# Optimization experiments

Hardware: AMD Instinct MI355X
Metric: run time of the kernel (lower is better)

## Reference

```python
import jax, jax.numpy as jnp
import numpy as np

EMBED_DIM = 1024
ATTN_DIM = 128
B, S = 4, 2048


def setup_inputs() -> dict:
    key = jax.random.key(0)
    k1, k2, k3, k4 = jax.random.split(key, 4)
    embedded = jax.random.normal(k1, (B, S, EMBED_DIM), dtype=jnp.float32)
    # torch nn.Linear weights are [out_features, in_features]
    scale = 1.0 / np.sqrt(EMBED_DIM)
    Wk = jax.random.uniform(k2, (ATTN_DIM, EMBED_DIM), dtype=jnp.float32, minval=-scale, maxval=scale)
    Wq = jax.random.uniform(k3, (ATTN_DIM, EMBED_DIM), dtype=jnp.float32, minval=-scale, maxval=scale)
    Wv = jax.random.uniform(k4, (ATTN_DIM, EMBED_DIM), dtype=jnp.float32, minval=-scale, maxval=scale)
    return {"embedded": embedded, "Wk": Wk, "Wq": Wq, "Wv": Wv}


def reference(embedded, Wk, Wq, Wv):
    # projections (no bias): x @ W.T
    k = jnp.einsum('bse,ae->bsa', embedded, Wk)  # [B,S,A]
    q = jnp.einsum('bse,ae->bsa', embedded, Wq)
    v = jnp.einsum('bse,ae->bsa', embedded, Wv)
    ad = k.shape[-1]
    scores = jnp.einsum('bqa,bka->bqk', q, k) / jnp.sqrt(jnp.float32(ad))  # [B,S,S]
    causal = jnp.tril(jnp.ones((scores.shape[1], scores.shape[1]), dtype=bool))
    scores = jnp.where(causal, scores, -jnp.inf)
    probs = jax.nn.softmax(scores, axis=-1)
    out = jnp.einsum('bqk,bka->bqa', probs, v)
    return jnp.round(out, 4)
```

## Files before the change

kernel.cpp:

```cpp
#include <hip/hip_runtime.h>
#include <hip/hip_bf16.h>
#include <math.h>

#define B 4
#define S 2048
#define E 1024
#define A 128
#define CHUNK 256
#define NCHMAX 8

typedef __attribute__((ext_vector_type(8))) short short8;
typedef __attribute__((ext_vector_type(4))) float floatx4;

static __device__ __forceinline__ short f2bf(float f) {
  union { float f; unsigned u; } c;
  c.f = f;
  unsigned r = (c.u + 0x7fffu + ((c.u >> 16) & 1u)) >> 16;
  return (short)r;
}
static __device__ __forceinline__ unsigned f2bf2(float x, float y) {
  __hip_bfloat162 h = __float22bfloat162_rn(float2{x, y});
  union { __hip_bfloat162 h; unsigned u; } c;
  c.h = h;
  return c.u;
}

__global__ __launch_bounds__(256) void proj_gemm(
    const float* __restrict__ X,
    const float* __restrict__ Wq,
    const float* __restrict__ Wk,
    const float* __restrict__ Wv,
    short* __restrict__ Qbf,
    short* __restrict__ Kbf,
    short* __restrict__ Vt) {
  __shared__ short As[64 * 64];
  __shared__ short Bs[128 * 64];

  const int m0 = blockIdx.x * 64;
  const int which = blockIdx.y;
  const float* Wpb = (which == 0) ? Wq : (which == 1) ? Wk : Wv;

  const int tid = threadIdx.x;
  const int wave = tid >> 6;
  const int lane = tid & 63;
  const int mh = wave & 1;
  const int nh = wave >> 1;
  const int l16 = lane & 15;
  const int quad = lane >> 4;

  int xbase[4], wbase[4], aoff[4], boff[4];
#pragma unroll
  for (int i = 0; i < 4; ++i) {
    const int fa = tid + i * 256;
    const int arow = fa >> 4, ac4 = fa & 15;
    xbase[i] = (m0 + arow) * E + ac4 * 4;
    aoff[i] = arow * 64 + (((ac4 >> 1) ^ (arow & 7)) << 3) + ((ac4 & 1) << 2);
    const int fb = tid + i * 256;
    const int brow = fb >> 3, bc8 = fb & 7;
    wbase[i] = brow * E + bc8 * 8;
    boff[i] = brow * 64 + ((bc8 ^ (brow & 7)) << 3);
  }

  int arb[2], brb[4], swz[2];
#pragma unroll
  for (int ms = 0; ms < 2; ++ms) arb[ms] = (mh * 32 + ms * 16 + l16) * 64;
#pragma unroll
  for (int nt = 0; nt < 4; ++nt) brb[nt] = (nh * 64 + nt * 16 + l16) * 64;
#pragma unroll
  for (int ks = 0; ks < 2; ++ks) swz[ks] = (((ks * 4 + quad) ^ (l16 & 7)) << 3);

  floatx4 acc[2][4] = {};
  float4 apl0[4], apl1[4];
  float4 bpl0[4][2], bpl1[4][2];

#pragma unroll
  for (int i = 0; i < 4; ++i) {
    apl0[i] = *(const float4*)&X[xbase[i]];
    bpl0[i][0] = *(const float4*)&Wpb[wbase[i]];
    bpl0[i][1] = *(const float4*)&Wpb[wbase[i] + 4];
    apl1[i] = *(const float4*)&X[xbase[i] + 64];
    bpl1[i][0] = *(const float4*)&Wpb[wbase[i] + 64];
    bpl1[i][1] = *(const float4*)&Wpb[wbase[i] + 68];
  }

#define PROJ_BODY(APL, BPL, KNEXT)                                            \
  do {                                                                        \
    __syncthreads();                                                          \
    _Pragma("unroll") for (int i = 0; i < 4; ++i) {                           \
      uint2 pk; pk.x = f2bf2(APL[i].x, APL[i].y);                             \
      pk.y = f2bf2(APL[i].z, APL[i].w);                                       \
      *(uint2*)&As[aoff[i]] = pk;                                             \
      uint4 pb;                                                               \
      pb.x = f2bf2(BPL[i][0].x, BPL[i][0].y);                                 \
      pb.y = f2bf2(BPL[i][0].z, BPL[i][0].w);                                 \
      pb.z = f2bf2(BPL[i][1].x, BPL[i][1].y);                                 \
      pb.w = f2bf2(BPL[i][1].z, BPL[i][1].w);                                 \
      *(uint4*)&Bs[boff[i]] = pb;                                             \
    }                                                                         \
    __syncthreads();                                                          \
    if ((KNEXT) < E) {                                                        \
      _Pragma("unroll") for (int i = 0; i < 4; ++i) {                         \
        APL[i] = *(const float4*)&X[xbase[i] + (KNEXT)];                      \
        BPL[i][0] = *(const float4*)&Wpb[wbase[i] + (KNEXT)];                 \
        BPL[i][1] = *(const float4*)&Wpb[wbase[i] + (KNEXT) + 4];             \
      }                                                                       \
    }                                                                         \
    short8 afr[2][2], bfr[4][2];                                              \
    _Pragma("unroll") for (int ms = 0; ms < 2; ++ms)                          \
      _Pragma("unroll") for (int ks = 0; ks < 2; ++ks)                        \
        afr[ms][ks] = *(const short8*)&As[arb[ms] + swz[ks]];                 \
    _Pragma("unroll") for (int nt = 0; nt < 4; ++nt)                          \
      _Pragma("unroll") for (int ks = 0; ks < 2; ++ks)                        \
        bfr[nt][ks] = *(const short8*)&Bs[brb[nt] + swz[ks]];                 \
    _Pragma("unroll") for (int ms = 0; ms < 2; ++ms)                          \
      _Pragma("unroll") for (int nt = 0; nt < 4; ++nt)                        \
        _Pragma("unroll") for (int ks = 0; ks < 2; ++ks)                      \
          acc[ms][nt] = __builtin_amdgcn_mfma_f32_16x16x32_bf16(              \
              afr[ms][ks], bfr[nt][ks], acc[ms][nt], 0, 0, 0);                \
  } while (0)

  for (int k0 = 0; k0 < E; k0 += 128) {
    PROJ_BODY(apl0, bpl0, k0 + 128);
    PROJ_BODY(apl1, bpl1, k0 + 192);
  }
#undef PROJ_BODY

  const float qscale = 0.08838834764831845f;
#pragma unroll
  for (int ms = 0; ms < 2; ++ms) {
#pragma unroll
    for (int nt = 0; nt < 4; ++nt) {
      const int n = nh * 64 + nt * 16 + l16;
      const int mbase = m0 + mh * 32 + ms * 16 + quad * 4;
      if (which == 2) {
        const int b = mbase >> 11, s = mbase & (S - 1);
        short4 p;
        p.x = f2bf(acc[ms][nt][0]); p.y = f2bf(acc[ms][nt][1]);
        p.z = f2bf(acc[ms][nt][2]); p.w = f2bf(acc[ms][nt][3]);
        *(short4*)&Vt[((size_t)b * A + n) * S + s] = p;
      } else {
        short* Outp = (which == 0) ? Qbf : Kbf;
        const float sc = (which == 0) ? qscale : 1.0f;
#pragma unroll
        for (int r = 0; r < 4; ++r)
          Outp[(size_t)(mbase + r) * A + n] = f2bf(acc[ms][nt][r] * sc);
      }
    }
  }
}

__global__ __launch_bounds__(256) void attn_part(
    const short* __restrict__ Qbf,
    const short* __restrict__ Kbf,
    const short* __restrict__ Vt,
    float* __restrict__ Opart,
    float* __restrict__ Lpart) {
  __shared__ short Ks[64 * 128];
  __shared__ short Vs[128 * 64];
  __shared__ short Ps[4][16 * 64];

  const int rev = (int)gridDim.x - 1 - (int)blockIdx.x;
  const int qt = rev >> 3;
  const int chunk = rev & 7;
  const int b = qt >> 5;
  const int q0 = (qt & 31) << 6;
  const int nk = q0 + 64;
  const int kstart = chunk * CHUNK;
  if (kstart >= nk) return;
  const int kend = min(kstart + CHUNK, nk);

  const int tid = threadIdx.x;
  const int wave = tid >> 6;
  const int lane = tid & 63;
  const int l16 = lane & 15;
  const int quad = lane >> 4;

  int kgb[4], vgb[4], kwoff[4], vwoff[4];
#pragma unroll
  for (int i = 0; i < 4; ++i) {
    const int f = tid + i * 256;
    const int krow = f >> 4, kc8 = f & 15;
    kgb[i] = krow * A + kc8 * 8;
    kwoff[i] = krow * 128 + ((kc8 ^ (krow & 7)) << 3);
    const int vrow = f >> 3, vc8 = f & 7;
    vgb[i] = vrow * S + vc8 * 8;
    vwoff[i] = vrow * 64 + ((vc8 ^ (vrow & 7)) << 3);
  }

  int swz[4];
#pragma unroll
  for (int ks = 0; ks < 4; ++ks) swz[ks] = (((ks * 4 + quad) ^ (l16 & 7)) << 3);

  int pwoff[4][4];
#pragma unroll
  for (int nt = 0; nt < 4; ++nt)
#pragma unroll
    for (int r = 0; r < 4; ++r) {
      const int row = quad * 4 + r;
      const int slot = nt * 2 + (l16 >> 3);
      pwoff[nt][r] = row * 64 + ((slot ^ (row & 7)) << 3) + (l16 & 7);
    }

  short8 qfr[4];
  {
    const size_t qrow = (size_t)(b * S + q0 + wave * 16 + l16);
#pragma unroll
    for (int ks = 0; ks < 4; ++ks)
      qfr[ks] = *(const short8*)&Qbf[qrow * A + ks * 32 + quad * 8];
  }

  float l_acc[4] = {0.f, 0.f, 0.f, 0.f};
  floatx4 oacc[8] = {};

  const int myrow = q0 + wave * 16 + quad * 4;
  const short* Kbase = Kbf + (size_t)b * S * A;
  const short* Vbase = Vt + (size_t)b * A * S;

  short8 kplf[4], vplf[4];
#pragma unroll
  for (int i = 0; i < 4; ++i) {
    kplf[i] = *(const short8*)&Kbase[kstart * A + kgb[i]];
    vplf[i] = *(const short8*)&Vbase[vgb[i] + kstart];
  }

  for (int j0 = kstart; j0 < kend; j0 += 64) {
    __syncthreads();
#pragma unroll
    for (int i = 0; i < 4; ++i) {
      *(short8*)&Ks[kwoff[i]] = kplf[i];
      *(short8*)&Vs[vwoff[i]] = vplf[i];
    }
    __syncthreads();

    if (j0 + 64 < kend) {
#pragma unroll
      for (int i = 0; i < 4; ++i) {
        kplf[i] = *(const short8*)&Kbase[(j0 + 64) * A + kgb[i]];
        vplf[i] = *(const short8*)&Vbase[vgb[i] + j0 + 64];
      }
    }

    floatx4 sc[4];
#pragma unroll
    for (int nt = 0; nt < 4; ++nt) {
      floatx4 c = {};
#pragma unroll
      for (int ks = 0; ks < 4; ++ks) {
        const short8 bfr = *(const short8*)&Ks[(nt * 16 + l16) * 128 + swz[ks]];
        c = __builtin_amdgcn_mfma_f32_16x16x32_bf16(qfr[ks], bfr, c, 0, 0, 0);
      }
      sc[nt] = c;
    }

#pragma unroll
    for (int nt = 0; nt < 4; ++nt) {
      const int key = j0 + nt * 16 + l16;
#pragma unroll
      for (int r = 0; r < 4; ++r) {
        const float p = (key > myrow + r) ? 0.f : __expf(sc[nt][r]);
        sc[nt][r] = p;
        l_acc[r] += p;
      }
    }

#pragma unroll
    for (int nt = 0; nt < 4; ++nt)
#pragma unroll
      for (int r = 0; r < 4; ++r)
        Ps[wave][pwoff[nt][r]] = f2bf(sc[nt][r]);

    short8 pfr[2];
#pragma unroll
    for (int ks = 0; ks < 2; ++ks)
      pfr[ks] = *(const short8*)&Ps[wave][l16 * 64 + swz[ks]];

#pragma unroll
    for (int nt = 0; nt < 8; ++nt) {
#pragma unroll
      for (int ks = 0; ks < 2; ++ks) {
        const short8 vfr = *(const short8*)&Vs[(nt * 16 + l16) * 64 + swz[ks]];
        oacc[nt] = __builtin_amdgcn_mfma_f32_16x16x32_bf16(pfr[ks], vfr, oacc[nt], 0, 0, 0);
      }
    }
  }

  const int slot = qt * NCHMAX + chunk;
  float* op = Opart + (size_t)slot * 64 * 128;
  const int lr = wave * 16 + quad * 4;
#pragma unroll
  for (int nt = 0; nt < 8; ++nt)
#pragma unroll
    for (int r = 0; r < 4; ++r)
      op[(lr + r) * 128 + nt * 16 + l16] = oacc[nt][r];

#pragma unroll
  for (int r = 0; r < 4; ++r) {
    float l = l_acc[r];
    l += __shfl_xor(l, 1);
    l += __shfl_xor(l, 2);
    l += __shfl_xor(l, 4);
    l += __shfl_xor(l, 8);
    if (l16 == 0) Lpart[slot * 64 + lr + r] = l;
  }
}

__global__ __launch_bounds__(256) void attn_reduce(
    const float* __restrict__ Opart,
    const float* __restrict__ Lpart,
    float* __restrict__ Out) {
  const int qt = blockIdx.x >> 2;
  const int quarter = blockIdx.x & 3;
  const int b = qt >> 5;
  const int q0 = (qt & 31) << 6;
  const int nch = (q0 + 64 + CHUNK - 1) / CHUNK;

  const int tid = threadIdx.x;
  const int lr = quarter * 16 + (tid >> 4);
  const int c0 = (tid & 15) * 8;

  float ltot = 0.f;
  for (int c = 0; c < nch; ++c) ltot += Lpart[(qt * NCHMAX + c) * 64 + lr];
  const float inv = 1.f / ltot;

  float4 acc[2] = {};
  for (int c = 0; c < nch; ++c) {
    const float4* op = (const float4*)
        (Opart + ((size_t)(qt * NCHMAX + c) * 64 + lr) * 128 + c0);
#pragma unroll
    for (int i = 0; i < 2; ++i) {
      const float4 v = op[i];
      acc[i].x += v.x; acc[i].y += v.y; acc[i].z += v.z; acc[i].w += v.w;
    }
  }

  float4* o = (float4*)(Out + (size_t)(b * S + q0 + lr) * A + c0);
#pragma unroll
  for (int i = 0; i < 2; ++i) {
    float4 v = acc[i];
    v.x *= inv; v.y *= inv; v.z *= inv; v.w *= inv;
    o[i] = v;
  }
}

extern "C" void kernel_launch(void* const* d_in, const int* in_sizes, int n_in,
                              void* d_out, int out_size, void* d_ws, size_t ws_size,
                              hipStream_t stream) {
  const float* X  = (const float*)d_in[0];
  const float* Wk = (const float*)d_in[1];
  const float* Wq = (const float*)d_in[2];
  const float* Wv = (const float*)d_in[3];
  float* Out = (float*)d_out;

  const size_t qkv_elems = (size_t)B * S * A;
  short* Qbf = (short*)d_ws;
  short* Kbf = Qbf + qkv_elems;
  short* Vt  = Kbf + qkv_elems;
  float* Opart = (float*)(Vt + qkv_elems);
  float* Lpart = Opart + (size_t)1024 * 64 * 128;

  dim3 pgrid(B * S / 64, 3);
  proj_gemm<<<pgrid, 256, 0, stream>>>(X, Wq, Wk, Wv, Qbf, Kbf, Vt);
  attn_part<<<(B * S / 64) * NCHMAX, 256, 0, stream>>>(Qbf, Kbf, Vt, Opart, Lpart);
  attn_reduce<<<B * S / 64 * 4, 256, 0, stream>>>(Opart, Lpart, Out);
}
```

Baseline: 124.1 us.

## Accumulate split-K attention partials with atomics instead of per-chunk buffers

Attention partial outputs and row sums are now accumulated into a single unnormalized output buffer with float atomicAdd, instead of being written to per-chunk slots and summed in the reduce kernel. The accumulators are zeroed inside the projection kernel. Query tiles that need only one key chunk write normalized output directly and skip the reduce. This cuts partial-buffer traffic and reduce work, at the cost of atomic contention and a nondeterministic summation order.

```diff
diff --git a/kernel.cpp b/kernel.cpp
--- a/kernel.cpp
+++ b/kernel.cpp
@@ -32,7 +32,9 @@
     const float* __restrict__ Wv,
     short* __restrict__ Qbf,
     short* __restrict__ Kbf,
-    short* __restrict__ Vt) {
+    short* __restrict__ Vt,
+    float* __restrict__ Ounn,
+    float* __restrict__ Ltot) {
   __shared__ short As[64 * 64];
   __shared__ short Bs[128 * 64];
 
@@ -41,6 +43,15 @@
   const float* Wpb = (which == 0) ? Wq : (which == 1) ? Wk : Wv;
 
   const int tid = threadIdx.x;
+
+  if (which == 0) {
+    const float4 z = {0.f, 0.f, 0.f, 0.f};
+    float4* zb = (float4*)&Ounn[(size_t)m0 * A];
+#pragma unroll
+    for (int i = 0; i < 8; ++i) zb[tid + i * 256] = z;
+    if (tid < 64) Ltot[m0 + tid] = 0.f;
+  }
+
   const int wave = tid >> 6;
   const int lane = tid & 63;
   const int mh = wave & 1;
@@ -153,8 +164,9 @@
     const short* __restrict__ Qbf,
     const short* __restrict__ Kbf,
     const short* __restrict__ Vt,
-    float* __restrict__ Opart,
-    float* __restrict__ Lpart) {
+    float* __restrict__ Ounn,
+    float* __restrict__ Ltot,
+    float* __restrict__ Out) {
   __shared__ short Ks[64 * 128];
   __shared__ short Vs[128 * 64];
   __shared__ short Ps[4][16 * 64];
@@ -168,6 +180,7 @@
   const int kstart = chunk * CHUNK;
   if (kstart >= nk) return;
   const int kend = min(kstart + CHUNK, nk);
+  const int nch = (nk + CHUNK - 1) / CHUNK;
 
   const int tid = threadIdx.x;
   const int wave = tid >> 6;
@@ -284,15 +297,8 @@
     }
   }
 
-  const int slot = qt * NCHMAX + chunk;
-  float* op = Opart + (size_t)slot * 64 * 128;
   const int lr = wave * 16 + quad * 4;
-#pragma unroll
-  for (int nt = 0; nt < 8; ++nt)
-#pragma unroll
-    for (int r = 0; r < 4; ++r)
-      op[(lr + r) * 128 + nt * 16 + l16] = oacc[nt][r];
-
+  float lsum[4];
 #pragma unroll
   for (int r = 0; r < 4; ++r) {
     float l = l_acc[r];
@@ -300,43 +306,59 @@
     l += __shfl_xor(l, 2);
     l += __shfl_xor(l, 4);
     l += __shfl_xor(l, 8);
-    if (l16 == 0) Lpart[slot * 64 + lr + r] = l;
+    lsum[r] = l;
+  }
+
+  if (nch == 1) {
+    float inv4[4];
+#pragma unroll
+    for (int r = 0; r < 4; ++r) inv4[r] = 1.f / lsum[r];
+    float* o = Out + (size_t)(b * S + q0 + lr) * A;
+#pragma unroll
+    for (int nt = 0; nt < 8; ++nt)
+#pragma unroll
+      for (int r = 0; r < 4; ++r)
+        o[(size_t)r * A + nt * 16 + l16] = oacc[nt][r] * inv4[r];
+    return;
+  }
+
+  float* orow = Ounn + (size_t)(b * S + q0 + lr) * A;
+#pragma unroll
+  for (int nt = 0; nt < 8; ++nt)
+#pragma unroll
+    for (int r = 0; r < 4; ++r)
+      atomicAdd(&orow[(size_t)r * A + nt * 16 + l16], oacc[nt][r]);
+
+  if (l16 == 0) {
+#pragma unroll
+    for (int r = 0; r < 4; ++r)
+      atomicAdd(&Ltot[b * S + q0 + lr + r], lsum[r]);
   }
 }
 
 __global__ __launch_bounds__(256) void attn_reduce(
-    const float* __restrict__ Opart,
-    const float* __restrict__ Lpart,
+    const float* __restrict__ Ounn,
+    const float* __restrict__ Ltot,
     float* __restrict__ Out) {
   const int qt = blockIdx.x >> 2;
   const int quarter = blockIdx.x & 3;
   const int b = qt >> 5;
   const int q0 = (qt & 31) << 6;
   const int nch = (q0 + 64 + CHUNK - 1) / CHUNK;
+  if (nch == 1) return;
 
   const int tid = threadIdx.x;
   const int lr = quarter * 16 + (tid >> 4);
   const int c0 = (tid & 15) * 8;
 
-  float ltot = 0.f;
-  for (int c = 0; c < nch; ++c) ltot += Lpart[(qt * NCHMAX + c) * 64 + lr];
-  const float inv = 1.f / ltot;
-
-  float4 acc[2] = {};
-  for (int c = 0; c < nch; ++c) {
-    const float4* op = (const float4*)
-        (Opart + ((size_t)(qt * NCHMAX + c) * 64 + lr) * 128 + c0);
-#pragma unroll
-    for (int i = 0; i < 2; ++i) {
-      const float4 v = op[i];
-      acc[i].x += v.x; acc[i].y += v.y; acc[i].z += v.z; acc[i].w += v.w;
-    }
-  }
-
-  float4* o = (float4*)(Out + (size_t)(b * S + q0 + lr) * A + c0);
+  const size_t row = (size_t)(b * S + q0 + lr);
+  const float inv = 1.f / Ltot[row];
+
+  const float4* src = (const float4*)(Ounn + row * A + c0);
+  float4* o = (float4*)(Out + row * A + c0);
 #pragma unroll
   for (int i = 0; i < 2; ++i) {
-    float4 v = acc[i];
+    float4 v = src[i];
     v.x *= inv; v.y *= inv; v.z *= inv; v.w *= inv;
     o[i] = v;
   }
@@ -355,11 +377,11 @@
   short* Qbf = (short*)d_ws;
   short* Kbf = Qbf + qkv_elems;
   short* Vt  = Kbf + qkv_elems;
-  float* Opart = (float*)(Vt + qkv_elems);
-  float* Lpart = Opart + (size_t)1024 * 64 * 128;
+  float* Ounn = (float*)(Vt + qkv_elems);
+  float* Ltot = Ounn + qkv_elems;
 
   dim3 pgrid(B * S / 64, 3);
-  proj_gemm<<<pgrid, 256, 0, stream>>>(X, Wq, Wk, Wv, Qbf, Kbf, Vt);
-  attn_part<<<(B * S / 64) * NCHMAX, 256, 0, stream>>>(Qbf, Kbf, Vt, Opart, Lpart);
-  attn_reduce<<<B * S / 64 * 4, 256, 0, stream>>>(Opart, Lpart, Out);
-}
+  proj_gemm<<<pgrid, 256, 0, stream>>>(X, Wq, Wk, Wv, Qbf, Kbf, Vt, Ounn, Ltot);
+  attn_part<<<(B * S / 64) * NCHMAX, 256, 0, stream>>>(Qbf, Kbf, Vt, Ounn, Ltot, Out);
+  attn_reduce<<<B * S / 64 * 4, 256, 0, stream>>>(Ounn, Ltot, Out);
+}
```

After: 123.7 us. No clear change (-0.3%).
